# Kernel tuning notes

Hardware: AMD Instinct MI355X
Metric: run time of the kernel (lower is better)

## Reference

```python
import jax, jax.numpy as jnp
import numpy as np

NUM_HEADS = 32
NUM_KV_HEADS = 8
NUM_GROUPS = NUM_HEADS // NUM_KV_HEADS  # 4
HEAD_DIM = 64
HIDDEN = 2048
ROPE_THETA = 10000.0


def rotate_half(x):
    half = x.shape[-1] // 2
    x1, x2 = x[..., :half], x[..., half:]
    return jnp.concatenate([-x2, x1], axis=-1)


def rope_cos_sin(seq_len, dtype):
    inv_freq = 1.0 / (ROPE_THETA ** (jnp.arange(0, HEAD_DIM, 2, dtype=jnp.float32) / HEAD_DIM))
    pos = jnp.arange(seq_len, dtype=jnp.float32)
    freqs = jnp.outer(pos, inv_freq)          # [S, HEAD_DIM/2]
    emb = jnp.concatenate([freqs, freqs], axis=-1)  # [S, HEAD_DIM]
    return jnp.cos(emb).astype(dtype), jnp.sin(emb).astype(dtype)


def setup_inputs() -> dict:
    key = jax.random.key(0)
    k0, k1, k2, k3, k4 = jax.random.split(key, 5)
    B, S = 2, 2048
    scale = 0.02
    return {
        "hidden_states": jax.random.normal(k0, (B, S, HIDDEN), dtype=jnp.float32),
        "Wq": jax.random.normal(k1, (NUM_HEADS * HEAD_DIM, HIDDEN), dtype=jnp.float32) * scale,
        "Wk": jax.random.normal(k2, (NUM_KV_HEADS * HEAD_DIM, HIDDEN), dtype=jnp.float32) * scale,
        "Wv": jax.random.normal(k3, (NUM_KV_HEADS * HEAD_DIM, HIDDEN), dtype=jnp.float32) * scale,
        "Wo": jax.random.normal(k4, (HIDDEN, NUM_HEADS * HEAD_DIM), dtype=jnp.float32) * scale,
    }


def reference(hidden_states, Wq, Wk, Wv, Wo):
    B, S, _ = hidden_states.shape
    # projections (nn.Linear: x @ W.T)
    q = (hidden_states @ Wq.T).reshape(B, S, NUM_HEADS, HEAD_DIM).transpose(0, 2, 1, 3)
    k = (hidden_states @ Wk.T).reshape(B, S, NUM_KV_HEADS, HEAD_DIM).transpose(0, 2, 1, 3)
    v = (hidden_states @ Wv.T).reshape(B, S, NUM_KV_HEADS, HEAD_DIM).transpose(0, 2, 1, 3)

    cos, sin = rope_cos_sin(S, q.dtype)  # [S, HEAD_DIM]
    cos = cos[None, None]                # [1,1,S,HEAD_DIM]
    sin = sin[None, None]
    q = q * cos + rotate_half(q) * sin
    k = k * cos + rotate_half(k) * sin

    # GQA: repeat kv heads to match query heads (repeat_interleave on head dim)
    k = jnp.repeat(k, NUM_GROUPS, axis=1)  # [B, NUM_HEADS, S, HEAD_DIM]
    v = jnp.repeat(v, NUM_GROUPS, axis=1)

    scale = 1.0 / jnp.sqrt(jnp.asarray(HEAD_DIM, dtype=q.dtype))
    scores = jnp.einsum('bhqd,bhkd->bhqk', q, k) * scale  # [B,H,S,S]
    causal = jnp.tril(jnp.ones((S, S), dtype=bool))
    scores = jnp.where(causal[None, None], scores, jnp.asarray(-jnp.inf, dtype=scores.dtype))
    attn = jax.nn.softmax(scores, axis=-1)
    out = jnp.einsum('bhqk,bhkd->bhqd', attn, v)           # [B,H,S,D]
    out = out.transpose(0, 2, 1, 3).reshape(B, S, NUM_HEADS * HEAD_DIM)
    return out @ Wo.T
```

## Files before the change

### kernel.cpp

```cpp
#include <hip/hip_runtime.h>

#define S_LEN 2048
#define BATCH 2
#define NH 32
#define NKV 8
#define HD 64
#define HID 2048
#define NTOK (BATCH * S_LEN)
#define NQKV 3072
#define SC_Q 0.18033688011112042f

typedef __attribute__((ext_vector_type(8))) __bf16 bf16x8;
typedef __attribute__((ext_vector_type(4))) float f32x4;
typedef __attribute__((ext_vector_type(4))) float f32x4v;
typedef __attribute__((ext_vector_type(4))) ushort u16x4;

__device__ inline ushort f2b(float f) {
    union { float f; unsigned u; } x{f};
    unsigned r = (x.u + 0x7fff + ((x.u >> 16) & 1)) >> 16;
    return (ushort)r;
}
__device__ inline float b2f(ushort u) {
    union { unsigned u; float f; } x{(unsigned)u << 16};
    return x.f;
}
__device__ inline float ex2(float x) { return __builtin_amdgcn_exp2f(x); }

__global__ __launch_bounds__(256) void cvt_all(const float* __restrict__ hidden,
                                               const float* __restrict__ Wq,
                                               const float* __restrict__ Wk,
                                               const float* __restrict__ Wv,
                                               const float* __restrict__ Wo,
                                               ushort* __restrict__ hb,
                                               ushort* __restrict__ wqkv,
                                               ushort* __restrict__ wo) {
    for (int bid = blockIdx.x; bid < 18432; bid += gridDim.x) {
        const float* src;
        ushort* dst;
        int off;
        if (bid < 8192)        { src = hidden; dst = hb;                              off = bid; }
        else if (bid < 12288)  { src = Wq;     dst = wqkv;                            off = bid - 8192; }
        else if (bid < 13312)  { src = Wk;     dst = wqkv + (size_t)2048 * 2048;      off = bid - 12288; }
        else if (bid < 14336)  { src = Wv;     dst = wqkv + (size_t)2560 * 2048;      off = bid - 13312; }
        else                   { src = Wo;     dst = wo;                              off = bid - 14336; }
        size_t i = (size_t)off * 256 + threadIdx.x;
        f32x4v v = __builtin_nontemporal_load((const f32x4v*)src + i);
        u16x4 o = {f2b(v[0]), f2b(v[1]), f2b(v[2]), f2b(v[3])};
        *((u16x4*)dst + i) = o;
    }
}

__device__ inline void gl_lds16(const void* g, void* l) {
    __builtin_amdgcn_global_load_lds((const __attribute__((address_space(1))) void*)g,
                                     (__attribute__((address_space(3))) void*)l, 16, 0, 0);
}

template<int CF, int WF32, int ROUTE>
__global__ __launch_bounds__(512, 2) void gemm8p(const ushort* __restrict__ A,
                                                 const ushort* __restrict__ B,
                                                 void* __restrict__ C,
                                                 ushort* __restrict__ Kd,
                                                 ushort* __restrict__ Vd,
                                                 int M, int N, int K) {
    constexpr int BN = CF * 64;
    constexpr int ABYTES = 256 * 64 * 2;
    constexpr int BBYTES = BN * 64 * 2;
    __shared__ __align__(16) char lds[2][ABYTES + BBYTES];
    const int tid = threadIdx.x, lane = tid & 63, w = tid >> 6;
    const int wm = w >> 2, wn = w & 3, l15 = lane & 15, lg = lane >> 4;

    const int nbx = gridDim.x;
    int lid = blockIdx.y * nbx + blockIdx.x;
    const int cpx = (nbx * gridDim.y) >> 3;
    int swzb = (lid & 7) * cpx + (lid >> 3);
    const int m0 = (swzb / nbx) * 256, n0 = (swzb % nbx) * BN;

    const int srow = tid >> 3;
    const int scol = ((tid & 7) ^ (srow & 7)) * 8;
    const ushort* Ag = A + (size_t)(m0 + srow) * K + scol;
    const ushort* Bg = B + (size_t)(n0 + srow) * K + scol;

    auto stage = [&](int buf, int k0) {
        char* base = &lds[buf][0];
#pragma unroll
        for (int j = 0; j < CF; j++)
            gl_lds16(Bg + (size_t)(j * 64) * K + k0, base + ABYTES + (j * 64 + w * 8) * 128);
        gl_lds16(Ag + k0,                      base + (0 * 64 + w * 8) * 128);
        gl_lds16(Ag + (size_t)(2 * 64) * K + k0, base + (2 * 64 + w * 8) * 128);
        gl_lds16(Ag + (size_t)(1 * 64) * K + k0, base + (1 * 64 + w * 8) * 128);
        gl_lds16(Ag + (size_t)(3 * 64) * K + k0, base + (3 * 64 + w * 8) * 128);
    };

    f32x4 acc[8][CF] = {};

    stage(0, 0);

    const int NT = K >> 6;
    const int sw = (l15 & 7) * 16;
    const int po0 = (lg * 16) ^ sw, po1 = (64 + lg * 16) ^ sw;

    for (int t = 0; t < NT; ++t) {
        const char* pa = &lds[t & 1][0] + (wm * 128 + l15) * 128;
        const char* pb = &lds[t & 1][ABYTES] + (wn * CF * 16 + l15) * 128;

        asm volatile("s_waitcnt vmcnt(2)" ::: "memory");
        __builtin_amdgcn_s_barrier();
        __builtin_amdgcn_sched_barrier(0);
        if (t + 1 < NT) stage((t + 1) & 1, (t + 1) << 6);
        __builtin_amdgcn_sched_barrier(0);

        bf16x8 bf_[2][CF];
#pragma unroll
        for (int j = 0; j < CF; j++) {
            bf_[0][j] = *(const bf16x8*)(pb + j * 2048 + po0);
            bf_[1][j] = *(const bf16x8*)(pb + j * 2048 + po1);
        }
        bf16x8 a_[2][4];
#pragma unroll
        for (int i = 0; i < 4; i++) {
            a_[0][i] = *(const bf16x8*)(pa + i * 2048 + po0);
            a_[1][i] = *(const bf16x8*)(pa + i * 2048 + po1);
        }
        __builtin_amdgcn_s_setprio(1);
#pragma unroll
        for (int ks = 0; ks < 2; ks++)
#pragma unroll
            for (int i = 0; i < 4; i++)
#pragma unroll
                for (int j = 0; j < CF; j++)
                    acc[i][j] = __builtin_amdgcn_mfma_f32_16x16x32_bf16(a_[ks][i], bf_[ks][j], acc[i][j], 0, 0, 0);
        __builtin_amdgcn_s_setprio(0);

        if (t < NT - 1) {
            if constexpr (CF == 3) asm volatile("s_waitcnt vmcnt(7)" ::: "memory");
            else                   asm volatile("s_waitcnt vmcnt(6)" ::: "memory");
        } else {
            asm volatile("s_waitcnt vmcnt(0)" ::: "memory");
        }
        __builtin_amdgcn_s_barrier();
        __builtin_amdgcn_sched_barrier(0);

        bf16x8 c_[2][4];
#pragma unroll
        for (int i = 0; i < 4; i++) {
            c_[0][i] = *(const bf16x8*)(pa + (4 + i) * 2048 + po0);
            c_[1][i] = *(const bf16x8*)(pa + (4 + i) * 2048 + po1);
        }
        __builtin_amdgcn_s_setprio(1);
#pragma unroll
        for (int ks = 0; ks < 2; ks++)
#pragma unroll
            for (int i = 0; i < 4; i++)
#pragma unroll
                for (int j = 0; j < CF; j++)
                    acc[4 + i][j] = __builtin_amdgcn_mfma_f32_16x16x32_bf16(c_[ks][i], bf_[ks][j], acc[4 + i][j], 0, 0, 0);
        __builtin_amdgcn_s_setprio(0);
    }

    const int mr = m0 + wm * 128 + lg * 4;

    if (ROUTE) {
#pragma unroll
        for (int j = 0; j < CF; j++) {
            int cb = n0 + wn * CF * 16 + j * 16;
            ushort* dst;
            int dstride, colb;
            if (cb < 2048)      { dst = (ushort*)C; dstride = 2048; colb = cb + l15; }
            else if (cb < 2560) { dst = Kd;         dstride = 512;  colb = cb - 2048 + l15; }
            else                { dst = Vd;         dstride = 512;  colb = cb - 2560 + l15; }
#pragma unroll
            for (int i = 0; i < 8; i++)
#pragma unroll
                for (int r = 0; r < 4; r++)
                    dst[(size_t)(mr + i * 16 + r) * dstride + colb] = f2b(acc[i][j][r]);
        }
    } else {
#pragma unroll
        for (int i = 0; i < 8; i++)
#pragma unroll
            for (int j = 0; j < CF; j++)
#pragma unroll
                for (int r = 0; r < 4; r++) {
                    size_t row = mr + i * 16 + r, col = n0 + wn * CF * 16 + j * 16 + l15;
                    if (WF32) ((float*)C)[row * N + col] = acc[i][j][r];
                    else      ((ushort*)C)[row * N + col] = f2b(acc[i][j][r]);
                }
    }
}

__global__ __launch_bounds__(256) void rope_k(ushort* __restrict__ Kb) {
    int idx = blockIdx.x * 256 + threadIdx.x;
    int t = idx >> 5, rem = idx & 31;
    int hh = rem >> 2, q8 = rem & 3;
    float pos = (float)(t & (S_LEN - 1));
    ushort* base = Kb + (size_t)t * 512 + hh * 64 + q8 * 8;
    ushort4 v0 = *(ushort4*)base, v1 = *(ushort4*)(base + 4);
    ushort4 u0 = *(ushort4*)(base + 32), u1 = *(ushort4*)(base + 36);
    ushort lo[8] = {v0.x, v0.y, v0.z, v0.w, v1.x, v1.y, v1.z, v1.w};
    ushort hi[8] = {u0.x, u0.y, u0.z, u0.w, u1.x, u1.y, u1.z, u1.w};
#pragma unroll
    for (int e = 0; e < 8; e++) {
        float f = ex2(-(float)(q8 * 8 + e) * 0.4152410118609203f);
        float sv, cv;
        __sincosf(pos * f, &sv, &cv);
        float x1 = b2f(lo[e]), x2 = b2f(hi[e]);
        lo[e] = f2b(x1 * cv - x2 * sv);
        hi[e] = f2b(x2 * cv + x1 * sv);
    }
    *(ushort4*)base        = make_ushort4(lo[0], lo[1], lo[2], lo[3]);
    *(ushort4*)(base + 4)  = make_ushort4(lo[4], lo[5], lo[6], lo[7]);
    *(ushort4*)(base + 32) = make_ushort4(hi[0], hi[1], hi[2], hi[3]);
    *(ushort4*)(base + 36) = make_ushort4(hi[4], hi[5], hi[6], hi[7]);
}

__global__ __launch_bounds__(256) void transpose_v(const ushort* __restrict__ V,
                                                   ushort* __restrict__ Vt) {
    __shared__ ushort tile[32][33];
    int bz = blockIdx.z, b = bz >> 3, kvh = bz & 7;
    int s0 = blockIdx.x * 32, d0 = blockIdx.y * 32;
    int tx = threadIdx.x & 31, ty = threadIdx.x >> 5;
#pragma unroll
    for (int i = 0; i < 4; i++)
        tile[ty + i * 8][tx] = V[(size_t)(b * S_LEN + s0 + ty + i * 8) * 512 + kvh * 64 + d0 + tx];
    __syncthreads();
#pragma unroll
    for (int i = 0; i < 4; i++)
        Vt[((size_t)((b * 8 + kvh) * 64 + d0 + ty + i * 8)) * S_LEN + s0 + tx] = tile[tx][ty + i * 8];
}

__global__ __launch_bounds__(256) void attn_k(const ushort* __restrict__ Q,
                                              const ushort* __restrict__ Kc,
                                              const ushort* __restrict__ Vt,
                                              ushort* __restrict__ O) {
    __shared__ __align__(16) ushort K_lds[3][4096];
    __shared__ __align__(16) ushort V_lds[3][4096];
    const int lane = threadIdx.x & 63, w = threadIdx.x >> 6;
    const int l15 = lane & 15, lg = lane >> 4;

    int lid = blockIdx.y * 8 + blockIdx.x;
    int swz = (lid & 7) * 64 + (lid >> 3);
    const int ps = swz & 7;
    const int bh = swz >> 3;
    const int b = bh >> 5, h = bh & 31, kvh = h >> 2;

    const ushort* kSrc[2];
    const ushort* vSrc[2];
    int dstU[2];
#pragma unroll
    for (int j = 0; j < 2; j++) {
        int u = w * 2 + j;
        int row = u * 8 + (lane >> 3);
        int po = (lane & 7) * 16;
        int fr = ((row & 3) | (((row >> 3) & 1) << 2)) << 4;
        int dus = (po ^ fr) >> 1;
        kSrc[j] = Kc + (size_t)(b * S_LEN + row) * 512 + kvh * 64 + dus;
        vSrc[j] = Vt + ((size_t)((b * 8 + kvh) * 64 + row)) * S_LEN + dus;
        dstU[j] = u * 512;
    }

    int fr_k = ((l15 & 3) | (((l15 >> 2) & 1) << 2)) << 4;
    int kbase = 1024 * (l15 >> 2) + 128 * (l15 & 3) + ((lg * 16) ^ (fr_k & 48));
    int k6 = (fr_k >> 6) & 1;
    int kb0 = kbase + 64 * k6, kb1 = kbase + 64 * (1 - k6);
    int fr_v = ((l15 & 3) | (((l15 >> 3) & 1) << 2)) << 4;
    int vbase = 128 * l15 + ((lg * 16) ^ (fr_v & 48));
    int v6 = (fr_v >> 6) & 1;
    int vb0 = vbase + 64 * v6, vb1 = vbase + 64 * (1 - v6);

    bf16x8 onesf;
#pragma unroll
    for (int i = 0; i < 8; i++) onesf[i] = (__bf16)1.0f;

    auto ropeq = [&](bf16x8& q0, bf16x8& q1, int qrow) {
        float pos = (float)qrow;
#pragma unroll
        for (int e = 0; e < 8; e++) {
            float f = ex2(-(float)(lg * 8 + e) * 0.4152410118609203f);
            float sv, cv;
            __sincosf(pos * f, &sv, &cv);
            float x1 = (float)q0[e], x2 = (float)q1[e];
            q0[e] = (__bf16)((x1 * cv - x2 * sv) * SC_Q);
            q1[e] = (__bf16)((x2 * cv + x1 * sv) * SC_Q);
        }
    };

    for (int half = 0; half < 2; ++half) {
        const int pp = half ? (15 - ps) : ps;
        const int q0A = pp * 128 + w * 16, q0B = q0A + 64;
        const int qrowA = q0A + l15, qrowB = q0B + l15;
        const int ktA = 2 * pp, ktB = 2 * pp + 1;

        const ushort* qpA = Q + (size_t)(b * S_LEN + qrowA) * HID + h * 64 + lg * 8;
        const ushort* qpB = Q + (size_t)(b * S_LEN + qrowB) * HID + h * 64 + lg * 8;
        bf16x8 qfA0 = *(const bf16x8*)qpA, qfA1 = *(const bf16x8*)(qpA + 32);
        bf16x8 qfB0 = *(const bf16x8*)qpB, qfB1 = *(const bf16x8*)(qpB + 32);
        ropeq(qfA0, qfA1, qrowA);
        ropeq(qfB0, qfB1, qrowB);
        asm volatile("s_waitcnt vmcnt(0)" ::: "memory");

        f32x4 aoA[4] = {}, aoB[4] = {};
        f32x4 lsumA = {}, lsumB = {};

        int i0 = 0, i1 = 1, i2 = 2;
#pragma unroll
        for (int j = 0; j < 2; j++) {
            gl_lds16(kSrc[j], &K_lds[0][dstU[j]]);
            gl_lds16(vSrc[j], &V_lds[0][dstU[j]]);
        }
#pragma unroll
        for (int j = 0; j < 2; j++) {
            gl_lds16(kSrc[j] + (size_t)64 * 512, &K_lds[1][dstU[j]]);
            gl_lds16(vSrc[j] + 64, &V_lds[1][dstU[j]]);
        }

        for (int kt = 0; kt <= ktB; ++kt) {
            const int kn = kt << 6;
            if (kt < ktB) asm volatile("s_waitcnt vmcnt(4)" ::: "memory");
            else          asm volatile("s_waitcnt vmcnt(0)" ::: "memory");
            __builtin_amdgcn_s_barrier();

            if (kt + 2 <= ktB) {
                const int kn2 = kn + 128;
#pragma unroll
                for (int j = 0; j < 2; j++) {
                    gl_lds16(kSrc[j] + (size_t)kn2 * 512, &K_lds[i2][dstU[j]]);
                    gl_lds16(vSrc[j] + kn2, &V_lds[i2][dstU[j]]);
                }
            }

            const char* Kt = (const char*)&K_lds[i0][0];
            const char* Vl = (const char*)&V_lds[i0][0];
            const bool aAct = (kt <= ktA);

            bf16x8 kf0[4], kf1[4];
#pragma unroll
            for (int kc = 0; kc < 4; kc++) {
                const int kcst = 4096 * (kc >> 1) + 512 * (kc & 1);
                kf0[kc] = *(const bf16x8*)(Kt + kb0 + kcst);
                kf1[kc] = *(const bf16x8*)(Kt + kb1 + kcst);
            }

            f32x4 sB[4], sA[4];
#pragma unroll
            for (int kc = 0; kc < 4; kc++) {
                f32x4 z = {};
                z = __builtin_amdgcn_mfma_f32_16x16x32_bf16(kf0[kc], qfB0, z, 0, 0, 0);
                z = __builtin_amdgcn_mfma_f32_16x16x32_bf16(kf1[kc], qfB1, z, 0, 0, 0);
                sB[kc] = z;
            }
            if (aAct) {
#pragma unroll
                for (int kc = 0; kc < 4; kc++) {
                    f32x4 z = {};
                    z = __builtin_amdgcn_mfma_f32_16x16x32_bf16(kf0[kc], qfA0, z, 0, 0, 0);
                    z = __builtin_amdgcn_mfma_f32_16x16x32_bf16(kf1[kc], qfA1, z, 0, 0, 0);
                    sA[kc] = z;
                }
            }

            if (kt == ktB) {
#pragma unroll
                for (int kc = 0; kc < 4; kc++)
#pragma unroll
                    for (int r = 0; r < 4; r++) {
                        int kv = kn + ((kc >> 1) << 5) + (lg << 3) + ((kc & 1) << 2) + r;
                        sB[kc][r] = (kv <= qrowB) ? sB[kc][r] : -INFINITY;
                    }
            }
            if (kt == ktA) {
#pragma unroll
                for (int kc = 0; kc < 4; kc++)
#pragma unroll
                    for (int r = 0; r < 4; r++) {
                        int kv = kn + ((kc >> 1) << 5) + (lg << 3) + ((kc & 1) << 2) + r;
                        sA[kc][r] = (kv <= qrowA) ? sA[kc][r] : -INFINITY;
                    }
            }

            bf16x8 pB0, pB1, pA0, pA1;
#pragma unroll
            for (int r = 0; r < 4; r++) {
                pB0[r]     = (__bf16)ex2(sB[0][r]);
                pB0[4 + r] = (__bf16)ex2(sB[1][r]);
                pB1[r]     = (__bf16)ex2(sB[2][r]);
                pB1[4 + r] = (__bf16)ex2(sB[3][r]);
            }
            if (aAct) {
#pragma unroll
                for (int r = 0; r < 4; r++) {
                    pA0[r]     = (__bf16)ex2(sA[0][r]);
                    pA0[4 + r] = (__bf16)ex2(sA[1][r]);
                    pA1[r]     = (__bf16)ex2(sA[2][r]);
                    pA1[4 + r] = (__bf16)ex2(sA[3][r]);
                }
            }

            lsumB = __builtin_amdgcn_mfma_f32_16x16x32_bf16(pB0, onesf, lsumB, 0, 0, 0);
            lsumB = __builtin_amdgcn_mfma_f32_16x16x32_bf16(pB1, onesf, lsumB, 0, 0, 0);
            if (aAct) {
                lsumA = __builtin_amdgcn_mfma_f32_16x16x32_bf16(pA0, onesf, lsumA, 0, 0, 0);
                lsumA = __builtin_amdgcn_mfma_f32_16x16x32_bf16(pA1, onesf, lsumA, 0, 0, 0);
            }

#pragma unroll
            for (int dt = 0; dt < 4; dt++) {
                bf16x8 vf0 = *(const bf16x8*)(Vl + vb0 + dt * 2048);
                bf16x8 vf1 = *(const bf16x8*)(Vl + vb1 + dt * 2048);
                aoB[dt] = __builtin_amdgcn_mfma_f32_16x16x32_bf16(pB0, vf0, aoB[dt], 0, 0, 0);
                aoB[dt] = __builtin_amdgcn_mfma_f32_16x16x32_bf16(pB1, vf1, aoB[dt], 0, 0, 0);
                if (aAct) {
                    aoA[dt] = __builtin_amdgcn_mfma_f32_16x16x32_bf16(pA0, vf0, aoA[dt], 0, 0, 0);
                    aoA[dt] = __builtin_amdgcn_mfma_f32_16x16x32_bf16(pA1, vf1, aoA[dt], 0, 0, 0);
                }
            }

            int t = i0; i0 = i1; i1 = i2; i2 = t;
        }

        float invA[4], invB[4];
#pragma unroll
        for (int r = 0; r < 4; r++) { invA[r] = 1.0f / lsumA[r]; invB[r] = 1.0f / lsumB[r]; }
        ushort* obA = O + (size_t)(b * S_LEN + q0A + lg * 4) * HID + h * 64 + l15;
        ushort* obB = O + (size_t)(b * S_LEN + q0B + lg * 4) * HID + h * 64 + l15;
#pragma unroll
        for (int dt = 0; dt < 4; dt++)
#pragma unroll
            for (int r = 0; r < 4; r++) {
                union { __bf16 h; ushort u; } cA{(__bf16)(aoA[dt][r] * invA[r])};
                union { __bf16 h; ushort u; } cB{(__bf16)(aoB[dt][r] * invB[r])};
                obA[(size_t)r * HID + dt * 16] = cA.u;
                obB[(size_t)r * HID + dt * 16] = cB.u;
            }

        __builtin_amdgcn_s_barrier();
    }
}

extern "C" void kernel_launch(void* const* d_in, const int* in_sizes, int n_in,
                              void* d_out, int out_size, void* d_ws, size_t ws_size,
                              hipStream_t stream) {
    const float* hidden = (const float*)d_in[0];
    const float* Wq = (const float*)d_in[1];
    const float* Wk = (const float*)d_in[2];
    const float* Wv = (const float*)d_in[3];
    const float* Wo = (const float*)d_in[4];

    char* ws = (char*)d_ws;
    size_t off = 0;
    auto alloc = [&](size_t bytes) -> void* {
        void* p = ws + off;
        off += (bytes + 255) & ~(size_t)255;
        return p;
    };
    ushort* hb   = (ushort*)alloc((size_t)NTOK * HID * 2);
    ushort* wqkv = (ushort*)alloc((size_t)NQKV * 2048 * 2);
    ushort* wo   = (ushort*)alloc((size_t)2048 * 2048 * 2);
    ushort* Qb   = (ushort*)alloc((size_t)NTOK * 2048 * 2);
    ushort* Kb   = (ushort*)alloc((size_t)NTOK * 512 * 2);
    ushort* Vb   = (ushort*)alloc((size_t)NTOK * 512 * 2);
    ushort* Vtb  = (ushort*)alloc((size_t)NTOK * 512 * 2);
    ushort* AO   = (ushort*)alloc((size_t)NTOK * 2048 * 2);

    cvt_all<<<2304, 256, 0, stream>>>(hidden, Wq, Wk, Wv, Wo, hb, wqkv, wo);

    gemm8p<3, 0, 1><<<dim3(16, 16), 512, 0, stream>>>(hb, wqkv, Qb, Kb, Vb, NTOK, NQKV, 2048);

    rope_k<<<(NTOK * 32) / 256, 256, 0, stream>>>(Kb);

    transpose_v<<<dim3(S_LEN / 32, 2, BATCH * NKV), 256, 0, stream>>>(Vb, Vtb);

    attn_k<<<dim3(8, BATCH * NH), 256, 0, stream>>>(Qb, Kb, Vtb, AO);

    gemm8p<2, 1, 0><<<dim3(16, 16), 512, 0, stream>>>(AO, wo, d_out, nullptr, nullptr, NTOK, 2048, 2048);
}
```

Measured before the change: 164.3 us.

## Split GEMM template and give output projection its own 128x256 tiled kernel

The shared templated GEMM is split into a QKV-specific kernel and a dedicated output-projection kernel. The output projection now uses 128x256 tiles (grid 8x32), a 64x64 per-wave subtile and a prefetch-two-stages pipeline that issues the next load after a barrier, replacing the 256x128 split-half schedule. The aim is better MFMA/LDS-read balance and more overlap of global loads with compute in the final GEMM. It adds code duplication and changes the wait counts, which need to match the new number of loads per stage.

```diff
diff --git a/kernel.cpp b/kernel.cpp
--- a/kernel.cpp
+++ b/kernel.cpp
@@ -55,16 +55,15 @@
                                      (__attribute__((address_space(3))) void*)l, 16, 0, 0);
 }
 
-template<int CF, int WF32, int ROUTE>
-__global__ __launch_bounds__(512, 2) void gemm8p(const ushort* __restrict__ A,
-                                                 const ushort* __restrict__ B,
-                                                 void* __restrict__ C,
-                                                 ushort* __restrict__ Kd,
-                                                 ushort* __restrict__ Vd,
-                                                 int M, int N, int K) {
-    constexpr int BN = CF * 64;
+__global__ __launch_bounds__(512, 2) void gemmQKV(const ushort* __restrict__ A,
+                                                  const ushort* __restrict__ B,
+                                                  ushort* __restrict__ Qd,
+                                                  ushort* __restrict__ Kd,
+                                                  ushort* __restrict__ Vd,
+                                                  int M, int N, int K) {
+    constexpr int CF = 3;
     constexpr int ABYTES = 256 * 64 * 2;
-    constexpr int BBYTES = BN * 64 * 2;
+    constexpr int BBYTES = 192 * 64 * 2;
     __shared__ __align__(16) char lds[2][ABYTES + BBYTES];
     const int tid = threadIdx.x, lane = tid & 63, w = tid >> 6;
     const int wm = w >> 2, wn = w & 3, l15 = lane & 15, lg = lane >> 4;
@@ -73,7 +72,7 @@
     int lid = blockIdx.y * nbx + blockIdx.x;
     const int cpx = (nbx * gridDim.y) >> 3;
     int swzb = (lid & 7) * cpx + (lid >> 3);
-    const int m0 = (swzb / nbx) * 256, n0 = (swzb % nbx) * BN;
+    const int m0 = (swzb / nbx) * 256, n0 = (swzb % nbx) * (CF * 64);
 
     const int srow = tid >> 3;
     const int scol = ((tid & 7) ^ (srow & 7)) * 8;
@@ -85,7 +84,7 @@
 #pragma unroll
         for (int j = 0; j < CF; j++)
             gl_lds16(Bg + (size_t)(j * 64) * K + k0, base + ABYTES + (j * 64 + w * 8) * 128);
-        gl_lds16(Ag + k0,                      base + (0 * 64 + w * 8) * 128);
+        gl_lds16(Ag + k0,                        base + (0 * 64 + w * 8) * 128);
         gl_lds16(Ag + (size_t)(2 * 64) * K + k0, base + (2 * 64 + w * 8) * 128);
         gl_lds16(Ag + (size_t)(1 * 64) * K + k0, base + (1 * 64 + w * 8) * 128);
         gl_lds16(Ag + (size_t)(3 * 64) * K + k0, base + (3 * 64 + w * 8) * 128);
@@ -131,12 +130,8 @@
                     acc[i][j] = __builtin_amdgcn_mfma_f32_16x16x32_bf16(a_[ks][i], bf_[ks][j], acc[i][j], 0, 0, 0);
         __builtin_amdgcn_s_setprio(0);
 
-        if (t < NT - 1) {
-            if constexpr (CF == 3) asm volatile("s_waitcnt vmcnt(7)" ::: "memory");
-            else                   asm volatile("s_waitcnt vmcnt(6)" ::: "memory");
-        } else {
-            asm volatile("s_waitcnt vmcnt(0)" ::: "memory");
-        }
+        if (t < NT - 1) asm volatile("s_waitcnt vmcnt(7)" ::: "memory");
+        else            asm volatile("s_waitcnt vmcnt(0)" ::: "memory");
         __builtin_amdgcn_s_barrier();
         __builtin_amdgcn_sched_barrier(0);
 
@@ -158,34 +153,102 @@
     }
 
     const int mr = m0 + wm * 128 + lg * 4;
-
-    if (ROUTE) {
-#pragma unroll
-        for (int j = 0; j < CF; j++) {
-            int cb = n0 + wn * CF * 16 + j * 16;
-            ushort* dst;
-            int dstride, colb;
-            if (cb < 2048)      { dst = (ushort*)C; dstride = 2048; colb = cb + l15; }
-            else if (cb < 2560) { dst = Kd;         dstride = 512;  colb = cb - 2048 + l15; }
-            else                { dst = Vd;         dstride = 512;  colb = cb - 2560 + l15; }
-#pragma unroll
-            for (int i = 0; i < 8; i++)
-#pragma unroll
-                for (int r = 0; r < 4; r++)
-                    dst[(size_t)(mr + i * 16 + r) * dstride + colb] = f2b(acc[i][j][r]);
-        }
-    } else {
+#pragma unroll
+    for (int j = 0; j < CF; j++) {
+        int cb = n0 + wn * CF * 16 + j * 16;
+        ushort* dst;
+        int dstride, colb;
+        if (cb < 2048)      { dst = Qd; dstride = 2048; colb = cb + l15; }
+        else if (cb < 2560) { dst = Kd; dstride = 512;  colb = cb - 2048 + l15; }
+        else                { dst = Vd; dstride = 512;  colb = cb - 2560 + l15; }
 #pragma unroll
         for (int i = 0; i < 8; i++)
 #pragma unroll
-            for (int j = 0; j < CF; j++)
-#pragma unroll
-                for (int r = 0; r < 4; r++) {
-                    size_t row = mr + i * 16 + r, col = n0 + wn * CF * 16 + j * 16 + l15;
-                    if (WF32) ((float*)C)[row * N + col] = acc[i][j][r];
-                    else      ((ushort*)C)[row * N + col] = f2b(acc[i][j][r]);
-                }
-    }
+            for (int r = 0; r < 4; r++)
+                dst[(size_t)(mr + i * 16 + r) * dstride + colb] = f2b(acc[i][j][r]);
+    }
+}
+
+__global__ __launch_bounds__(512, 2) void gemmO(const ushort* __restrict__ A,
+                                                const ushort* __restrict__ B,
+                                                float* __restrict__ C,
+                                                int M, int N, int K) {
+    constexpr int ABYTES = 128 * 64 * 2;
+    constexpr int BBYTES = 256 * 64 * 2;
+    __shared__ __align__(16) char lds[2][ABYTES + BBYTES];
+    const int tid = threadIdx.x, lane = tid & 63, w = tid >> 6;
+    const int wm = w >> 2, wn = w & 3, l15 = lane & 15, lg = lane >> 4;
+
+    const int nbx = gridDim.x;
+    int lid = blockIdx.y * nbx + blockIdx.x;
+    const int cpx = (nbx * gridDim.y) >> 3;
+    int swzb = (lid & 7) * cpx + (lid >> 3);
+    const int m0 = (swzb / nbx) * 128, n0 = (swzb % nbx) * 256;
+
+    const int srow = tid >> 3;
+    const int scol = ((tid & 7) ^ (srow & 7)) * 8;
+    const ushort* Ag = A + (size_t)(m0 + srow) * K + scol;
+    const ushort* Bg = B + (size_t)(n0 + srow) * K + scol;
+
+    auto stage = [&](int buf, int k0) {
+        char* base = &lds[buf][0];
+        gl_lds16(Ag + k0,                   base + (w * 8) * 128);
+        gl_lds16(Ag + (size_t)64 * K + k0,  base + (64 + w * 8) * 128);
+#pragma unroll
+        for (int j = 0; j < 4; j++)
+            gl_lds16(Bg + (size_t)(j * 64) * K + k0, base + ABYTES + (j * 64 + w * 8) * 128);
+    };
+
+    f32x4 acc[4][4] = {};
+
+    stage(0, 0);
+    stage(1, 64);
+
+    const int NT = K >> 6;
+    const int sw = (l15 & 7) * 16;
+    const int po0 = (lg * 16) ^ sw, po1 = (64 + lg * 16) ^ sw;
+
+    for (int t = 0; t < NT; ++t) {
+        if (t < NT - 1) asm volatile("s_waitcnt vmcnt(6)" ::: "memory");
+        else            asm volatile("s_waitcnt vmcnt(0)" ::: "memory");
+        __builtin_amdgcn_s_barrier();
+        __builtin_amdgcn_sched_barrier(0);
+
+        const char* pa = &lds[t & 1][0] + (wm * 64 + l15) * 128;
+        const char* pb = &lds[t & 1][ABYTES] + (wn * 64 + l15) * 128;
+
+        bf16x8 a_[2][4], b_[2][4];
+#pragma unroll
+        for (int i = 0; i < 4; i++) {
+            a_[0][i] = *(const bf16x8*)(pa + i * 2048 + po0);
+            a_[1][i] = *(const bf16x8*)(pa + i * 2048 + po1);
+            b_[0][i] = *(const bf16x8*)(pb + i * 2048 + po0);
+            b_[1][i] = *(const bf16x8*)(pb + i * 2048 + po1);
+        }
+        __builtin_amdgcn_s_setprio(1);
+#pragma unroll
+        for (int ks = 0; ks < 2; ks++)
+#pragma unroll
+            for (int i = 0; i < 4; i++)
+#pragma unroll
+                for (int j = 0; j < 4; j++)
+                    acc[i][j] = __builtin_amdgcn_mfma_f32_16x16x32_bf16(a_[ks][i], b_[ks][j], acc[i][j], 0, 0, 0);
+        __builtin_amdgcn_s_setprio(0);
+
+        __builtin_amdgcn_sched_barrier(0);
+        __builtin_amdgcn_s_barrier();
+        __builtin_amdgcn_sched_barrier(0);
+        if (t + 2 < NT) stage(t & 1, (t + 2) << 6);
+    }
+
+    const int mr = m0 + wm * 64 + lg * 4, nc = n0 + wn * 64 + l15;
+#pragma unroll
+    for (int i = 0; i < 4; i++)
+#pragma unroll
+        for (int j = 0; j < 4; j++)
+#pragma unroll
+            for (int r = 0; r < 4; r++)
+                C[(size_t)(mr + i * 16 + r) * N + nc + j * 16] = acc[i][j][r];
 }
 
 __global__ __launch_bounds__(256) void rope_k(ushort* __restrict__ Kb) {
@@ -463,7 +526,7 @@
 
     cvt_all<<<2304, 256, 0, stream>>>(hidden, Wq, Wk, Wv, Wo, hb, wqkv, wo);
 
-    gemm8p<3, 0, 1><<<dim3(16, 16), 512, 0, stream>>>(hb, wqkv, Qb, Kb, Vb, NTOK, NQKV, 2048);
+    gemmQKV<<<dim3(16, 16), 512, 0, stream>>>(hb, wqkv, Qb, Kb, Vb, NTOK, NQKV, 2048);
 
     rope_k<<<(NTOK * 32) / 256, 256, 0, stream>>>(Kb);
 
@@ -471,5 +534,5 @@
 
     attn_k<<<dim3(8, BATCH * NH), 256, 0, stream>>>(Qb, Kb, Vtb, AO);
 
-    gemm8p<2, 1, 0><<<dim3(16, 16), 512, 0, stream>>>(AO, wo, d_out, nullptr, nullptr, NTOK, 2048, 2048);
-}
+    gemmO<<<dim3(8, 32), 512, 0, stream>>>(AO, wo, (float*)d_out, NTOK, 2048, 2048);
+}
```

Result: no change. 166.8 us (+1.5%).
